# Optimization experiments

Hardware: AMD Instinct MI355X
Metric: run time of the kernel (lower is better)

Reference implementation:

```python
import jax, jax.numpy as jnp
import numpy as np
from jax import lax

B, H, W = 512, 128, 128
ARCH = [1, 4096, 4096, 4096, 4096]
CONV_THRESH = 0.0
GRAPH_THRESH = 0.8
EMBED_DIM = 1


def setup_inputs() -> dict:
    key = jax.random.key(0)
    ks = jax.random.split(key, 16)
    inp = {
        "x": jax.random.normal(ks[0], (B, 1, H, W), dtype=jnp.float32),
        "conv_w": jax.random.normal(ks[1], (1, 1, 2, 2), dtype=jnp.float32) * 0.5,
        "conv_b": jax.random.normal(ks[2], (1,), dtype=jnp.float32) * 0.1,
        "rotation": jax.random.normal(ks[3], (EMBED_DIM, EMBED_DIM), dtype=jnp.float32),
        "entangle": jax.random.normal(ks[4], (EMBED_DIM, EMBED_DIM), dtype=jnp.float32),
    }
    # Linear params, torch convention W: [out_f, in_f]
    for i, (fi, fo) in enumerate(zip(ARCH[:-1], ARCH[1:])):
        inp[f"W{i+1}"] = jax.random.normal(ks[5 + 2 * i], (fo, fi), dtype=jnp.float32) / np.sqrt(fi)
        inp[f"b{i+1}"] = jax.random.normal(ks[6 + 2 * i], (fo,), dtype=jnp.float32) * 0.01
    return inp


def _forward(x, conv_w, conv_b, rotation, entangle, W1, b1, W2, b2, W3, b3, W4, b4):
    # ConvFilter: 2x2 valid conv, sigmoid(logits - thresh), mean over C,H,W -> [B]
    logits = lax.conv_general_dilated(
        x, conv_w, window_strides=(1, 1), padding="VALID",
        dimension_numbers=("NCHW", "OIHW", "NCHW"))
    logits = logits + conv_b.reshape(1, -1, 1, 1)
    conv_out = jax.nn.sigmoid(logits - CONV_THRESH).mean(axis=(1, 2, 3))  # [B]
    conv_vec = conv_out[:, None]  # [B, 1] -> embed_dim forced to 1

    # ClassicalSelfAttention (embed_dim = 1)
    q = conv_vec @ rotation                      # [B, 1]
    k = conv_vec @ entangle                      # [B, 1]
    scores = jax.nn.softmax((q @ k.T) / np.sqrt(EMBED_DIM).astype(np.float32), axis=-1)  # [B, B]
    attn_out = scores @ conv_vec                 # [B, 1]

    # tanh MLP stack
    out = attn_out
    acts = []
    for Wl, bl in ((W1, b1), (W2, b2), (W3, b3), (W4, b4)):
        out = jnp.tanh(out @ Wl.T + bl)          # [B, out_f]
        acts.append(out)

    # Vectorized fidelity adjacency over equal-shaped layer activations:
    # normalized Gram matrix squared, thresholded (replaces the O(L^2)
    # Python loop with .item() syncs in the source).
    S = jnp.stack([a.reshape(-1) for a in acts])                  # [L, B*4096]
    S_hat = S / (jnp.linalg.norm(S, axis=1, keepdims=True) + 1e-12)
    fid = (S_hat @ S_hat.T) ** 2                                   # [L, L]
    L = len(acts)
    weights = jnp.where(fid >= GRAPH_THRESH, 1.0, 0.0) * (1.0 - jnp.eye(L, dtype=fid.dtype))
    return out, weights


def reference(x, conv_w, conv_b, rotation, entangle, W1, b1, W2, b2, W3, b3, W4, b4):
    return _forward(x, conv_w, conv_b, rotation, entangle, W1, b1, W2, b2, W3, b3, W4, b4)
```

## Files before the change

### kernel.cpp

```cpp
#include <hip/hip_runtime.h>
#include <cmath>


#define NEL (512 * 4096)

typedef float  floatx4 __attribute__((ext_vector_type(4)));
typedef _Float16 halfx8 __attribute__((ext_vector_type(8)));

__global__ __launch_bounds__(256) void conv_mean_kernel(
    const float* __restrict__ x, const float* __restrict__ cw,
    const float* __restrict__ cb, float* __restrict__ c_out)
{
  __shared__ float sbuf[4];
  const int b = blockIdx.x;
  const float w00 = cw[0], w01 = cw[1], w10 = cw[2], w11 = cw[3];
  const float bias = cb[0];
  const float* xb = x + (size_t)b * 128 * 128;
  float acc = 0.f;
  for (int t = threadIdx.x; t < 127 * 32; t += 256) {
    const int i  = t >> 5;
    const int j0 = (t & 31) << 2;
    const float* pr0 = xb + i * 128 + j0;
    const float* pr1 = pr0 + 128;
    const float4 a4 = *reinterpret_cast<const float4*>(pr0);
    const float  a5 = pr0[4];
    const float4 b4 = *reinterpret_cast<const float4*>(pr1);
    const float  b5 = pr1[4];
    const float a[5] = {a4.x, a4.y, a4.z, a4.w, a5};
    const float bb[5] = {b4.x, b4.y, b4.z, b4.w, b5};
    #pragma unroll
    for (int m = 0; m < 4; ++m) {
      if (j0 + m < 127) {
        float v = w00 * a[m] + w01 * a[m + 1] + w10 * bb[m] + w11 * bb[m + 1] + bias;
        acc += 1.0f / (1.0f + __expf(-v));
      }
    }
  }
  #pragma unroll
  for (int off = 32; off > 0; off >>= 1) acc += __shfl_down(acc, off, 64);
  const int lane = threadIdx.x & 63, wv = threadIdx.x >> 6;
  if (lane == 0) sbuf[wv] = acc;
  __syncthreads();
  if (threadIdx.x == 0)
    c_out[b] = (sbuf[0] + sbuf[1] + sbuf[2] + sbuf[3]) * (1.0f / 16129.0f);
}

__global__ __launch_bounds__(64) void attn_kernel(
    const float* __restrict__ c, const float* __restrict__ rot,
    const float* __restrict__ ent, float* __restrict__ attn)
{
  const int i = blockIdx.x;
  const int lane = threadIdx.x;
  const float t = rot[0] * ent[0] * c[i];
  float vals[8], cj[8];
  float mx = -1e30f;
  #pragma unroll
  for (int u = 0; u < 8; ++u) {
    float cv = c[lane + u * 64];
    cj[u] = cv;
    vals[u] = t * cv;
    mx = fmaxf(mx, vals[u]);
  }
  #pragma unroll
  for (int off = 32; off > 0; off >>= 1) mx = fmaxf(mx, __shfl_down(mx, off, 64));
  mx = __shfl(mx, 0, 64);
  float se = 0.f, sw = 0.f;
  #pragma unroll
  for (int u = 0; u < 8; ++u) {
    float e = __expf(vals[u] - mx);
    se += e;
    sw += e * cj[u];
  }
  #pragma unroll
  for (int off = 32; off > 0; off >>= 1) {
    se += __shfl_down(se, off, 64);
    sw += __shfl_down(sw, off, 64);
  }
  if (lane == 0) attn[i] = sw / se;
}

__global__ __launch_bounds__(256) void layer1_kernel(
    const float* __restrict__ attn, const float* __restrict__ W1,
    const float* __restrict__ b1, float* __restrict__ act1)
{
  const int o = blockIdx.x * 256 + threadIdx.x;
  const int i = blockIdx.y;
  act1[(size_t)i * 4096 + o] = tanhf(attn[i] * W1[o] + b1[o]);
}

#define BM 128
#define BN 128
#define BK 32
#define LDK 40

template<bool FUSE>
__global__ __launch_bounds__(256, 4) void gemm_tanh_kernel(
    const float* __restrict__ A, const float* __restrict__ W,
    const float* __restrict__ bias, float* __restrict__ C)
{
  __shared__ _Float16 As[2][BM][LDK];
  __shared__ _Float16 Ws[2][BN][LDK];
  const int K = 4096, N = 4096;
  const int tid  = threadIdx.x;
  const int lane = tid & 63;
  const int wave = tid >> 6;
  const int wm = (wave >> 1) * 64;
  const int wn = (wave & 1) * 64;
  const int q  = lane >> 4;
  const int ml = lane & 15;
  const int tileM = blockIdx.y * BM;
  const int tileN = blockIdx.x * BN;
  const int Kslice = K / gridDim.z;
  const int kbeg = blockIdx.z * Kslice;
  const int kend = kbeg + Kslice;
  float* Cb = FUSE ? C : C + (size_t)blockIdx.z * NEL;

  floatx4 acc[4][4] = {};

  const int r0  = tid >> 2;
  const int cc0 = (tid & 3) << 3;

  float4 pa[4], pw[4];
  auto load_tile = [&](int k0) {
    #pragma unroll
    for (int u = 0; u < 2; ++u) {
      const float* ap = A + (size_t)(tileM + r0 + u * 64) * K + k0 + cc0;
      pa[2 * u]     = *reinterpret_cast<const float4*>(ap);
      pa[2 * u + 1] = *reinterpret_cast<const float4*>(ap + 4);
      const float* wp = W + (size_t)(tileN + r0 + u * 64) * K + k0 + cc0;
      pw[2 * u]     = *reinterpret_cast<const float4*>(wp);
      pw[2 * u + 1] = *reinterpret_cast<const float4*>(wp + 4);
    }
  };
  auto store_tile = [&](int buf) {
    #pragma unroll
    for (int u = 0; u < 2; ++u) {
      halfx8 ha = { (_Float16)pa[2*u].x, (_Float16)pa[2*u].y,
                    (_Float16)pa[2*u].z, (_Float16)pa[2*u].w,
                    (_Float16)pa[2*u+1].x, (_Float16)pa[2*u+1].y,
                    (_Float16)pa[2*u+1].z, (_Float16)pa[2*u+1].w };
      *reinterpret_cast<halfx8*>(&As[buf][r0 + u * 64][cc0]) = ha;
      halfx8 hw = { (_Float16)pw[2*u].x, (_Float16)pw[2*u].y,
                    (_Float16)pw[2*u].z, (_Float16)pw[2*u].w,
                    (_Float16)pw[2*u+1].x, (_Float16)pw[2*u+1].y,
                    (_Float16)pw[2*u+1].z, (_Float16)pw[2*u+1].w };
      *reinterpret_cast<halfx8*>(&Ws[buf][r0 + u * 64][cc0]) = hw;
    }
  };

  load_tile(kbeg);
  store_tile(0);
  int cur = 0;

  for (int k0 = kbeg; k0 < kend; k0 += BK) {
    const bool more = (k0 + BK < kend);
    if (more) load_tile(k0 + BK);
    __syncthreads();

    halfx8 af[4], bf[4];
    #pragma unroll
    for (int i = 0; i < 4; ++i)
      af[i] = *reinterpret_cast<const halfx8*>(&As[cur][wm + i * 16 + ml][q * 8]);
    #pragma unroll
    for (int j = 0; j < 4; ++j)
      bf[j] = *reinterpret_cast<const halfx8*>(&Ws[cur][wn + j * 16 + ml][q * 8]);

    #pragma unroll
    for (int i = 0; i < 4; ++i)
      #pragma unroll
      for (int j = 0; j < 4; ++j)
        acc[i][j] = __builtin_amdgcn_mfma_f32_16x16x32_f16(af[i], bf[j], acc[i][j], 0, 0, 0);

    if (more) store_tile(cur ^ 1);
    cur ^= 1;
  }

  #pragma unroll
  for (int i = 0; i < 4; ++i) {
    const int row0 = tileM + wm + i * 16 + q * 4;
    #pragma unroll
    for (int j = 0; j < 4; ++j) {
      const int col = tileN + wn + j * 16 + ml;
      if (FUSE) {
        const float bv = bias[col];
        #pragma unroll
        for (int r = 0; r < 4; ++r)
          Cb[(size_t)(row0 + r) * N + col] = tanhf(acc[i][j][r] + bv);
      } else {
        #pragma unroll
        for (int r = 0; r < 4; ++r)
          Cb[(size_t)(row0 + r) * N + col] = acc[i][j][r];
      }
    }
  }
}

template<int S>
__global__ __launch_bounds__(256) void combine_tanh_kernel(
    const float* __restrict__ part, const float* __restrict__ bias,
    float* __restrict__ outp)
{
  const int i4 = blockIdx.x * 256 + threadIdx.x;
  const floatx4* p4 = (const floatx4*)part;
  floatx4 s = p4[i4];
  #pragma unroll
  for (int z = 1; z < S; ++z) s += p4[(size_t)z * (NEL / 4) + i4];
  const floatx4 bv = ((const floatx4*)bias)[i4 & 1023];
  floatx4 o;
  #pragma unroll
  for (int r = 0; r < 4; ++r) o[r] = tanhf(s[r] + bv[r]);
  ((floatx4*)outp)[i4] = o;
}

__global__ __launch_bounds__(256) void fid_dots_kernel(
    const float* __restrict__ a1, const float* __restrict__ a2,
    const float* __restrict__ a3, const float* __restrict__ a4,
    float* __restrict__ D)
{
  __shared__ float sred[4][10];
  float s[10] = {0, 0, 0, 0, 0, 0, 0, 0, 0, 0};
  const int n4 = NEL / 4;
  const int stride = gridDim.x * blockDim.x;
  const floatx4* p1 = (const floatx4*)a1;
  const floatx4* p2 = (const floatx4*)a2;
  const floatx4* p3 = (const floatx4*)a3;
  const floatx4* p4 = (const floatx4*)a4;
  for (int i = blockIdx.x * 256 + threadIdx.x; i < n4; i += stride) {
    floatx4 v1 = p1[i], v2 = p2[i], v3 = p3[i], v4 = p4[i];
    #pragma unroll
    for (int r = 0; r < 4; ++r) {
      s[0] += v1[r] * v1[r]; s[1] += v1[r] * v2[r]; s[2] += v1[r] * v3[r];
      s[3] += v1[r] * v4[r]; s[4] += v2[r] * v2[r]; s[5] += v2[r] * v3[r];
      s[6] += v2[r] * v4[r]; s[7] += v3[r] * v3[r]; s[8] += v3[r] * v4[r];
      s[9] += v4[r] * v4[r];
    }
  }
  const int lane = threadIdx.x & 63, wv = threadIdx.x >> 6;
  #pragma unroll
  for (int p = 0; p < 10; ++p) {
    float v = s[p];
    #pragma unroll
    for (int off = 32; off > 0; off >>= 1) v += __shfl_down(v, off, 64);
    if (lane == 0) sred[wv][p] = v;
  }
  __syncthreads();
  if (threadIdx.x < 10) {
    float v = sred[0][threadIdx.x] + sred[1][threadIdx.x] +
              sred[2][threadIdx.x] + sred[3][threadIdx.x];
    atomicAdd(&D[threadIdx.x * 16], v);
  }
}

__global__ void finalize_kernel(const float* __restrict__ D, float* __restrict__ wout)
{
  const int i = threadIdx.x;
  if (i >= 16) return;
  const int p = i >> 2, qq = i & 3;
  const int a = p < qq ? p : qq;
  const int b = p < qq ? qq : p;
  const int base[4] = {0, 4, 7, 9};
  const float dpq = D[(base[a] + (b - a)) * 16];
  const float npv = sqrtf(D[base[p] * 16]) + 1e-12f;
  const float nqv = sqrtf(D[base[qq] * 16]) + 1e-12f;
  const float ch = dpq / (npv * nqv);
  const float fid = ch * ch;
  wout[i] = (fid >= 0.8f && p != qq) ? 1.0f : 0.0f;
}

extern "C" void kernel_launch(void* const* d_in, const int* in_sizes, int n_in,
                              void* d_out, int out_size, void* d_ws, size_t ws_size,
                              hipStream_t stream)
{
  const float* x   = (const float*)d_in[0];
  const float* cw  = (const float*)d_in[1];
  const float* cb  = (const float*)d_in[2];
  const float* rot = (const float*)d_in[3];
  const float* ent = (const float*)d_in[4];
  const float* W1  = (const float*)d_in[5];
  const float* b1  = (const float*)d_in[6];
  const float* W2  = (const float*)d_in[7];
  const float* b2  = (const float*)d_in[8];
  const float* W3  = (const float*)d_in[9];
  const float* b3  = (const float*)d_in[10];
  const float* W4  = (const float*)d_in[11];
  const float* b4  = (const float*)d_in[12];
  float* out = (float*)d_out;

  char*  ws    = (char*)d_ws;
  float* c_buf = (float*)(ws + 0);
  float* attn  = (float*)(ws + 2048);
  float* D     = (float*)(ws + 4096);
  float* act1  = (float*)(ws + 8192);
  float* act2  = act1 + NEL;
  float* act3  = act2 + NEL;
  float* part  = act3 + NEL;
  float* wout  = out + NEL;

  const size_t base_need = 8192 + (size_t)3 * NEL * 4;
  const bool sk8 = ws_size >= base_need + (size_t)8 * NEL * 4;
  const bool sk4 = ws_size >= base_need + (size_t)4 * NEL * 4;

  hipMemsetAsync(D, 0, 10 * 16 * sizeof(float), stream);
  conv_mean_kernel<<<512, 256, 0, stream>>>(x, cw, cb, c_buf);
  attn_kernel<<<512, 64, 0, stream>>>(c_buf, rot, ent, attn);
  layer1_kernel<<<dim3(16, 512), 256, 0, stream>>>(attn, W1, b1, act1);

  const int cgrid = NEL / 4 / 256;
  if (sk8) {
    dim3 g(4096 / BN, 512 / BM, 8);
    gemm_tanh_kernel<false><<<g, 256, 0, stream>>>(act1, W2, nullptr, part);
    combine_tanh_kernel<8><<<cgrid, 256, 0, stream>>>(part, b2, act2);
    gemm_tanh_kernel<false><<<g, 256, 0, stream>>>(act2, W3, nullptr, part);
    combine_tanh_kernel<8><<<cgrid, 256, 0, stream>>>(part, b3, act3);
    gemm_tanh_kernel<false><<<g, 256, 0, stream>>>(act3, W4, nullptr, part);
    combine_tanh_kernel<8><<<cgrid, 256, 0, stream>>>(part, b4, out);
  } else if (sk4) {
    dim3 g(4096 / BN, 512 / BM, 4);
    gemm_tanh_kernel<false><<<g, 256, 0, stream>>>(act1, W2, nullptr, part);
    combine_tanh_kernel<4><<<cgrid, 256, 0, stream>>>(part, b2, act2);
    gemm_tanh_kernel<false><<<g, 256, 0, stream>>>(act2, W3, nullptr, part);
    combine_tanh_kernel<4><<<cgrid, 256, 0, stream>>>(part, b3, act3);
    gemm_tanh_kernel<false><<<g, 256, 0, stream>>>(act3, W4, nullptr, part);
    combine_tanh_kernel<4><<<cgrid, 256, 0, stream>>>(part, b4, out);
  } else {
    dim3 g(4096 / BN, 512 / BM, 1);
    gemm_tanh_kernel<true><<<g, 256, 0, stream>>>(act1, W2, b2, act2);
    gemm_tanh_kernel<true><<<g, 256, 0, stream>>>(act2, W3, b3, act3);
    gemm_tanh_kernel<true><<<g, 256, 0, stream>>>(act3, W4, b4, out);
  }

  fid_dots_kernel<<<256, 256, 0, stream>>>(act1, act2, act3, out, D);
  finalize_kernel<<<1, 64, 0, stream>>>(D, wout);
}
```

Before: 422.7 us.

## Load GEMM operands directly from global into registers with fp16 activation copies

The GEMM kernel no longer stages tiles through LDS. Each wave loads its MFMA fragments straight from global memory, register double-buffered over two k-steps. The earlier layers now also write an fp16 copy of each activation, so the A operand is read at half the bytes. The 8-way split-K path is removed in favour of a 4-way split, and launch bounds drop to 2 blocks per CU. The aim is to cut LDS traffic and barriers, at the cost of extra fp16 stores, uncoalesced strided row reads across lanes, more register pressure, and lost tile reuse within each block.

Result: slower. 517.3 us (+22.4%).

```diff
diff --git a/kernel.cpp b/kernel.cpp
--- a/kernel.cpp
+++ b/kernel.cpp
@@ -6,6 +6,7 @@
 
 typedef float  floatx4 __attribute__((ext_vector_type(4)));
 typedef _Float16 halfx8 __attribute__((ext_vector_type(8)));
+typedef _Float16 halfx4 __attribute__((ext_vector_type(4)));
 
 __global__ __launch_bounds__(256) void conv_mean_kernel(
     const float* __restrict__ x, const float* __restrict__ cw,
@@ -81,26 +82,23 @@
 
 __global__ __launch_bounds__(256) void layer1_kernel(
     const float* __restrict__ attn, const float* __restrict__ W1,
-    const float* __restrict__ b1, float* __restrict__ act1)
+    const float* __restrict__ b1, float* __restrict__ act1,
+    _Float16* __restrict__ a1h)
 {
   const int o = blockIdx.x * 256 + threadIdx.x;
   const int i = blockIdx.y;
-  act1[(size_t)i * 4096 + o] = tanhf(attn[i] * W1[o] + b1[o]);
-}
-
-#define BM 128
-#define BN 128
-#define BK 32
-#define LDK 40
+  const float v = tanhf(attn[i] * W1[o] + b1[o]);
+  act1[(size_t)i * 4096 + o] = v;
+  a1h[(size_t)i * 4096 + o] = (_Float16)v;
+}
 
 template<bool FUSE>
-__global__ __launch_bounds__(256, 4) void gemm_tanh_kernel(
-    const float* __restrict__ A, const float* __restrict__ W,
-    const float* __restrict__ bias, float* __restrict__ C)
-{
-  __shared__ _Float16 As[2][BM][LDK];
-  __shared__ _Float16 Ws[2][BN][LDK];
-  const int K = 4096, N = 4096;
+__global__ __launch_bounds__(256, 2) void gemm_direct_kernel(
+    const _Float16* __restrict__ A16, const float* __restrict__ W,
+    const float* __restrict__ bias, float* __restrict__ C,
+    _Float16* __restrict__ Ch)
+{
+  constexpr int K = 4096, N = 4096;
   const int tid  = threadIdx.x;
   const int lane = tid & 63;
   const int wave = tid >> 6;
@@ -108,71 +106,57 @@
   const int wn = (wave & 1) * 64;
   const int q  = lane >> 4;
   const int ml = lane & 15;
-  const int tileM = blockIdx.y * BM;
-  const int tileN = blockIdx.x * BN;
+  const int tileM = blockIdx.y * 128;
+  const int tileN = blockIdx.x * 128;
   const int Kslice = K / gridDim.z;
   const int kbeg = blockIdx.z * Kslice;
   const int kend = kbeg + Kslice;
   float* Cb = FUSE ? C : C + (size_t)blockIdx.z * NEL;
 
+  const _Float16* Abase = A16 + (size_t)(tileM + wm + ml) * K + q * 8;
+  const float*    Wbase = W   + (size_t)(tileN + wn + ml) * K + q * 8;
+
   floatx4 acc[4][4] = {};
-
-  const int r0  = tid >> 2;
-  const int cc0 = (tid & 3) << 3;
-
-  float4 pa[4], pw[4];
-  auto load_tile = [&](int k0) {
-    #pragma unroll
-    for (int u = 0; u < 2; ++u) {
-      const float* ap = A + (size_t)(tileM + r0 + u * 64) * K + k0 + cc0;
-      pa[2 * u]     = *reinterpret_cast<const float4*>(ap);
-      pa[2 * u + 1] = *reinterpret_cast<const float4*>(ap + 4);
-      const float* wp = W + (size_t)(tileN + r0 + u * 64) * K + k0 + cc0;
-      pw[2 * u]     = *reinterpret_cast<const float4*>(wp);
-      pw[2 * u + 1] = *reinterpret_cast<const float4*>(wp + 4);
+  halfx8 af0[4], af1[4];
+  float4 wf0[4][2], wf1[4][2];
+
+  auto loadA = [&](halfx8 (&af)[4], int k0) {
+    #pragma unroll
+    for (int i = 0; i < 4; ++i)
+      af[i] = *reinterpret_cast<const halfx8*>(Abase + (size_t)i * 16 * K + k0);
+  };
+  auto loadW = [&](float4 (&wf)[4][2], int k0) {
+    #pragma unroll
+    for (int j = 0; j < 4; ++j) {
+      const float* p = Wbase + (size_t)j * 16 * K + k0;
+      wf[j][0] = *reinterpret_cast<const float4*>(p);
+      wf[j][1] = *reinterpret_cast<const float4*>(p + 4);
     }
   };
-  auto store_tile = [&](int buf) {
-    #pragma unroll
-    for (int u = 0; u < 2; ++u) {
-      halfx8 ha = { (_Float16)pa[2*u].x, (_Float16)pa[2*u].y,
-                    (_Float16)pa[2*u].z, (_Float16)pa[2*u].w,
-                    (_Float16)pa[2*u+1].x, (_Float16)pa[2*u+1].y,
-                    (_Float16)pa[2*u+1].z, (_Float16)pa[2*u+1].w };
-      *reinterpret_cast<halfx8*>(&As[buf][r0 + u * 64][cc0]) = ha;
-      halfx8 hw = { (_Float16)pw[2*u].x, (_Float16)pw[2*u].y,
-                    (_Float16)pw[2*u].z, (_Float16)pw[2*u].w,
-                    (_Float16)pw[2*u+1].x, (_Float16)pw[2*u+1].y,
-                    (_Float16)pw[2*u+1].z, (_Float16)pw[2*u+1].w };
-      *reinterpret_cast<halfx8*>(&Ws[buf][r0 + u * 64][cc0]) = hw;
-    }
-  };
-
-  load_tile(kbeg);
-  store_tile(0);
-  int cur = 0;
-
-  for (int k0 = kbeg; k0 < kend; k0 += BK) {
-    const bool more = (k0 + BK < kend);
-    if (more) load_tile(k0 + BK);
-    __syncthreads();
-
-    halfx8 af[4], bf[4];
-    #pragma unroll
-    for (int i = 0; i < 4; ++i)
-      af[i] = *reinterpret_cast<const halfx8*>(&As[cur][wm + i * 16 + ml][q * 8]);
+  auto consume = [&](halfx8 (&af)[4], float4 (&wf)[4][2]) {
+    halfx8 bf[4];
     #pragma unroll
     for (int j = 0; j < 4; ++j)
-      bf[j] = *reinterpret_cast<const halfx8*>(&Ws[cur][wn + j * 16 + ml][q * 8]);
-
+      bf[j] = halfx8{ (_Float16)wf[j][0].x, (_Float16)wf[j][0].y,
+                      (_Float16)wf[j][0].z, (_Float16)wf[j][0].w,
+                      (_Float16)wf[j][1].x, (_Float16)wf[j][1].y,
+                      (_Float16)wf[j][1].z, (_Float16)wf[j][1].w };
     #pragma unroll
     for (int i = 0; i < 4; ++i)
       #pragma unroll
       for (int j = 0; j < 4; ++j)
         acc[i][j] = __builtin_amdgcn_mfma_f32_16x16x32_f16(af[i], bf[j], acc[i][j], 0, 0, 0);
-
-    if (more) store_tile(cur ^ 1);
-    cur ^= 1;
+  };
+
+  loadA(af0, kbeg);
+  loadW(wf0, kbeg);
+  for (int k0 = kbeg; k0 < kend; k0 += 64) {
+    const bool m1 = (k0 + 32) < kend;
+    const bool m2 = (k0 + 64) < kend;
+    if (m1) { loadA(af1, k0 + 32); loadW(wf1, k0 + 32); }
+    consume(af0, wf0);
+    if (m2) { loadA(af0, k0 + 64); loadW(wf0, k0 + 64); }
+    if (m1) consume(af1, wf1);
   }
 
   #pragma unroll
@@ -184,8 +168,11 @@
       if (FUSE) {
         const float bv = bias[col];
         #pragma unroll
-        for (int r = 0; r < 4; ++r)
-          Cb[(size_t)(row0 + r) * N + col] = tanhf(acc[i][j][r] + bv);
+        for (int r = 0; r < 4; ++r) {
+          const float v = tanhf(acc[i][j][r] + bv);
+          Cb[(size_t)(row0 + r) * N + col] = v;
+          if (Ch) Ch[(size_t)(row0 + r) * N + col] = (_Float16)v;
+        }
       } else {
         #pragma unroll
         for (int r = 0; r < 4; ++r)
@@ -195,10 +182,10 @@
   }
 }
 
-template<int S>
+template<int S, bool H>
 __global__ __launch_bounds__(256) void combine_tanh_kernel(
     const float* __restrict__ part, const float* __restrict__ bias,
-    float* __restrict__ outp)
+    float* __restrict__ outp, _Float16* __restrict__ houtp)
 {
   const int i4 = blockIdx.x * 256 + threadIdx.x;
   const floatx4* p4 = (const floatx4*)part;
@@ -210,6 +197,10 @@
   #pragma unroll
   for (int r = 0; r < 4; ++r) o[r] = tanhf(s[r] + bv[r]);
   ((floatx4*)outp)[i4] = o;
+  if (H) {
+    halfx4 h = { (_Float16)o[0], (_Float16)o[1], (_Float16)o[2], (_Float16)o[3] };
+    ((halfx4*)houtp)[i4] = h;
+  }
 }
 
 __global__ __launch_bounds__(256) void fid_dots_kernel(
@@ -293,40 +284,34 @@
   float* act1  = (float*)(ws + 8192);
   float* act2  = act1 + NEL;
   float* act3  = act2 + NEL;
-  float* part  = act3 + NEL;
+  _Float16* a1h = (_Float16*)(act3 + NEL);
+  _Float16* a2h = a1h + NEL;
+  _Float16* a3h = a2h + NEL;
+  float* part  = (float*)(a3h + NEL);
   float* wout  = out + NEL;
 
-  const size_t base_need = 8192 + (size_t)3 * NEL * 4;
-  const bool sk8 = ws_size >= base_need + (size_t)8 * NEL * 4;
+  const size_t base_need = 8192 + (size_t)3 * NEL * 4 + (size_t)3 * NEL * 2;
   const bool sk4 = ws_size >= base_need + (size_t)4 * NEL * 4;
 
   hipMemsetAsync(D, 0, 10 * 16 * sizeof(float), stream);
   conv_mean_kernel<<<512, 256, 0, stream>>>(x, cw, cb, c_buf);
   attn_kernel<<<512, 64, 0, stream>>>(c_buf, rot, ent, attn);
-  layer1_kernel<<<dim3(16, 512), 256, 0, stream>>>(attn, W1, b1, act1);
+  layer1_kernel<<<dim3(16, 512), 256, 0, stream>>>(attn, W1, b1, act1, a1h);
 
   const int cgrid = NEL / 4 / 256;
-  if (sk8) {
-    dim3 g(4096 / BN, 512 / BM, 8);
-    gemm_tanh_kernel<false><<<g, 256, 0, stream>>>(act1, W2, nullptr, part);
-    combine_tanh_kernel<8><<<cgrid, 256, 0, stream>>>(part, b2, act2);
-    gemm_tanh_kernel<false><<<g, 256, 0, stream>>>(act2, W3, nullptr, part);
-    combine_tanh_kernel<8><<<cgrid, 256, 0, stream>>>(part, b3, act3);
-    gemm_tanh_kernel<false><<<g, 256, 0, stream>>>(act3, W4, nullptr, part);
-    combine_tanh_kernel<8><<<cgrid, 256, 0, stream>>>(part, b4, out);
-  } else if (sk4) {
-    dim3 g(4096 / BN, 512 / BM, 4);
-    gemm_tanh_kernel<false><<<g, 256, 0, stream>>>(act1, W2, nullptr, part);
-    combine_tanh_kernel<4><<<cgrid, 256, 0, stream>>>(part, b2, act2);
-    gemm_tanh_kernel<false><<<g, 256, 0, stream>>>(act2, W3, nullptr, part);
-    combine_tanh_kernel<4><<<cgrid, 256, 0, stream>>>(part, b3, act3);
-    gemm_tanh_kernel<false><<<g, 256, 0, stream>>>(act3, W4, nullptr, part);
-    combine_tanh_kernel<4><<<cgrid, 256, 0, stream>>>(part, b4, out);
+  if (sk4) {
+    dim3 g(32, 4, 4);
+    gemm_direct_kernel<false><<<g, 256, 0, stream>>>(a1h, W2, nullptr, part, nullptr);
+    combine_tanh_kernel<4, true><<<cgrid, 256, 0, stream>>>(part, b2, act2, a2h);
+    gemm_direct_kernel<false><<<g, 256, 0, stream>>>(a2h, W3, nullptr, part, nullptr);
+    combine_tanh_kernel<4, true><<<cgrid, 256, 0, stream>>>(part, b3, act3, a3h);
+    gemm_direct_kernel<false><<<g, 256, 0, stream>>>(a3h, W4, nullptr, part, nullptr);
+    combine_tanh_kernel<4, false><<<cgrid, 256, 0, stream>>>(part, b4, out, nullptr);
   } else {
-    dim3 g(4096 / BN, 512 / BM, 1);
-    gemm_tanh_kernel<true><<<g, 256, 0, stream>>>(act1, W2, b2, act2);
-    gemm_tanh_kernel<true><<<g, 256, 0, stream>>>(act2, W3, b3, act3);
-    gemm_tanh_kernel<true><<<g, 256, 0, stream>>>(act3, W4, b4, out);
+    dim3 g(32, 4, 1);
+    gemm_direct_kernel<true><<<g, 256, 0, stream>>>(a1h, W2, b2, act2, a2h);
+    gemm_direct_kernel<true><<<g, 256, 0, stream>>>(a2h, W3, b3, act3, a3h);
+    gemm_direct_kernel<true><<<g, 256, 0, stream>>>(a3h, W4, b4, out, nullptr);
   }
 
   fid_dots_kernel<<<256, 256, 0, stream>>>(act1, act2, act3, out, D);
```

## Swizzle LDS tiles, fuse attention with layer1, hardcode split-K 8 path

Applied to the files above, without the earlier changes.

Replaces the padded LDS layout (LDK 40) with an unpadded XOR-swizzled layout, shrinking shared memory while avoiding bank conflicts on the MFMA fragment reads. Replaces __syncthreads with an explicit lgkmcnt wait plus s_barrier, so the barrier no longer waits on outstanding global prefetch loads. Fuses the attention softmax and the layer-1 tanh into one kernel, removing a launch and the attn round trip. The workspace-size fallbacks are dropped and split-K 8 is hardcoded, which could fault if the workspace is smaller than that path needs.

After: 423.5 us. No clear change (+0.2%).

```diff
diff --git a/kernel.cpp b/kernel.cpp
--- a/kernel.cpp
+++ b/kernel.cpp
@@ -6,6 +6,11 @@
 
 typedef float  floatx4 __attribute__((ext_vector_type(4)));
 typedef _Float16 halfx8 __attribute__((ext_vector_type(8)));
+
+#define BM 128
+#define BN 128
+#define BK 32
+#define LDK 32
 
 __global__ __launch_bounds__(256) void conv_mean_kernel(
     const float* __restrict__ x, const float* __restrict__ cw,
@@ -45,58 +50,54 @@
     c_out[b] = (sbuf[0] + sbuf[1] + sbuf[2] + sbuf[3]) * (1.0f / 16129.0f);
 }
 
-__global__ __launch_bounds__(64) void attn_kernel(
+__global__ __launch_bounds__(256) void attn_layer1_kernel(
     const float* __restrict__ c, const float* __restrict__ rot,
-    const float* __restrict__ ent, float* __restrict__ attn)
-{
+    const float* __restrict__ ent, const float* __restrict__ W1,
+    const float* __restrict__ b1, float* __restrict__ act1)
+{
+  __shared__ float sattn;
   const int i = blockIdx.x;
-  const int lane = threadIdx.x;
-  const float t = rot[0] * ent[0] * c[i];
-  float vals[8], cj[8];
-  float mx = -1e30f;
-  #pragma unroll
-  for (int u = 0; u < 8; ++u) {
-    float cv = c[lane + u * 64];
-    cj[u] = cv;
-    vals[u] = t * cv;
-    mx = fmaxf(mx, vals[u]);
-  }
-  #pragma unroll
-  for (int off = 32; off > 0; off >>= 1) mx = fmaxf(mx, __shfl_down(mx, off, 64));
-  mx = __shfl(mx, 0, 64);
-  float se = 0.f, sw = 0.f;
-  #pragma unroll
-  for (int u = 0; u < 8; ++u) {
-    float e = __expf(vals[u] - mx);
-    se += e;
-    sw += e * cj[u];
-  }
-  #pragma unroll
-  for (int off = 32; off > 0; off >>= 1) {
-    se += __shfl_down(se, off, 64);
-    sw += __shfl_down(sw, off, 64);
-  }
-  if (lane == 0) attn[i] = sw / se;
-}
-
-__global__ __launch_bounds__(256) void layer1_kernel(
-    const float* __restrict__ attn, const float* __restrict__ W1,
-    const float* __restrict__ b1, float* __restrict__ act1)
-{
-  const int o = blockIdx.x * 256 + threadIdx.x;
-  const int i = blockIdx.y;
-  act1[(size_t)i * 4096 + o] = tanhf(attn[i] * W1[o] + b1[o]);
-}
-
-#define BM 128
-#define BN 128
-#define BK 32
-#define LDK 40
-
-template<bool FUSE>
-__global__ __launch_bounds__(256, 4) void gemm_tanh_kernel(
+  if (threadIdx.x < 64) {
+    const int lane = threadIdx.x;
+    const float t = rot[0] * ent[0] * c[i];
+    float vals[8], cj[8];
+    float mx = -1e30f;
+    #pragma unroll
+    for (int u = 0; u < 8; ++u) {
+      float cv = c[lane + u * 64];
+      cj[u] = cv;
+      vals[u] = t * cv;
+      mx = fmaxf(mx, vals[u]);
+    }
+    #pragma unroll
+    for (int off = 32; off > 0; off >>= 1) mx = fmaxf(mx, __shfl_down(mx, off, 64));
+    mx = __shfl(mx, 0, 64);
+    float se = 0.f, sw = 0.f;
+    #pragma unroll
+    for (int u = 0; u < 8; ++u) {
+      float e = __expf(vals[u] - mx);
+      se += e;
+      sw += e * cj[u];
+    }
+    #pragma unroll
+    for (int off = 32; off > 0; off >>= 1) {
+      se += __shfl_down(se, off, 64);
+      sw += __shfl_down(sw, off, 64);
+    }
+    if (lane == 0) sattn = sw / se;
+  }
+  __syncthreads();
+  const float av = sattn;
+  #pragma unroll
+  for (int k = 0; k < 16; ++k) {
+    const int o = k * 256 + threadIdx.x;
+    act1[(size_t)i * 4096 + o] = tanhf(av * W1[o] + b1[o]);
+  }
+}
+
+__global__ __launch_bounds__(256, 4) void gemm_kernel(
     const float* __restrict__ A, const float* __restrict__ W,
-    const float* __restrict__ bias, float* __restrict__ C)
+    float* __restrict__ part)
 {
   __shared__ _Float16 As[2][BM][LDK];
   __shared__ _Float16 Ws[2][BN][LDK];
@@ -110,24 +111,25 @@
   const int ml = lane & 15;
   const int tileM = blockIdx.y * BM;
   const int tileN = blockIdx.x * BN;
-  const int Kslice = K / gridDim.z;
-  const int kbeg = blockIdx.z * Kslice;
-  const int kend = kbeg + Kslice;
-  float* Cb = FUSE ? C : C + (size_t)blockIdx.z * NEL;
+  const int kbeg = blockIdx.z * 512;
+  const int kend = kbeg + 512;
+  float* Cb = part + (size_t)blockIdx.z * NEL;
 
   floatx4 acc[4][4] = {};
 
-  const int r0  = tid >> 2;
-  const int cc0 = (tid & 3) << 3;
+  const int r0 = tid >> 2;
+  const int u0 = tid & 3;
+  const int su0 = (u0 ^ (r0 & 3)) << 3;
+  const int sq = (q ^ (ml & 3)) << 3;
 
   float4 pa[4], pw[4];
   auto load_tile = [&](int k0) {
     #pragma unroll
     for (int u = 0; u < 2; ++u) {
-      const float* ap = A + (size_t)(tileM + r0 + u * 64) * K + k0 + cc0;
+      const float* ap = A + (size_t)(tileM + r0 + u * 64) * K + k0 + u0 * 8;
       pa[2 * u]     = *reinterpret_cast<const float4*>(ap);
       pa[2 * u + 1] = *reinterpret_cast<const float4*>(ap + 4);
-      const float* wp = W + (size_t)(tileN + r0 + u * 64) * K + k0 + cc0;
+      const float* wp = W + (size_t)(tileN + r0 + u * 64) * K + k0 + u0 * 8;
       pw[2 * u]     = *reinterpret_cast<const float4*>(wp);
       pw[2 * u + 1] = *reinterpret_cast<const float4*>(wp + 4);
     }
@@ -139,12 +141,12 @@
                     (_Float16)pa[2*u].z, (_Float16)pa[2*u].w,
                     (_Float16)pa[2*u+1].x, (_Float16)pa[2*u+1].y,
                     (_Float16)pa[2*u+1].z, (_Float16)pa[2*u+1].w };
-      *reinterpret_cast<halfx8*>(&As[buf][r0 + u * 64][cc0]) = ha;
+      *reinterpret_cast<halfx8*>(&As[buf][r0 + u * 64][su0]) = ha;
       halfx8 hw = { (_Float16)pw[2*u].x, (_Float16)pw[2*u].y,
                     (_Float16)pw[2*u].z, (_Float16)pw[2*u].w,
                     (_Float16)pw[2*u+1].x, (_Float16)pw[2*u+1].y,
                     (_Float16)pw[2*u+1].z, (_Float16)pw[2*u+1].w };
-      *reinterpret_cast<halfx8*>(&Ws[buf][r0 + u * 64][cc0]) = hw;
+      *reinterpret_cast<halfx8*>(&Ws[buf][r0 + u * 64][su0]) = hw;
     }
   };
 
@@ -155,15 +157,17 @@
   for (int k0 = kbeg; k0 < kend; k0 += BK) {
     const bool more = (k0 + BK < kend);
     if (more) load_tile(k0 + BK);
-    __syncthreads();
+
+    asm volatile("s_waitcnt lgkmcnt(0)" ::: "memory");
+    __builtin_amdgcn_s_barrier();
 
     halfx8 af[4], bf[4];
     #pragma unroll
     for (int i = 0; i < 4; ++i)
-      af[i] = *reinterpret_cast<const halfx8*>(&As[cur][wm + i * 16 + ml][q * 8]);
+      af[i] = *reinterpret_cast<const halfx8*>(&As[cur][wm + i * 16 + ml][sq]);
     #pragma unroll
     for (int j = 0; j < 4; ++j)
-      bf[j] = *reinterpret_cast<const halfx8*>(&Ws[cur][wn + j * 16 + ml][q * 8]);
+      bf[j] = *reinterpret_cast<const halfx8*>(&Ws[cur][wn + j * 16 + ml][sq]);
 
     #pragma unroll
     for (int i = 0; i < 4; ++i)
@@ -181,21 +185,13 @@
     #pragma unroll
     for (int j = 0; j < 4; ++j) {
       const int col = tileN + wn + j * 16 + ml;
-      if (FUSE) {
-        const float bv = bias[col];
-        #pragma unroll
-        for (int r = 0; r < 4; ++r)
-          Cb[(size_t)(row0 + r) * N + col] = tanhf(acc[i][j][r] + bv);
-      } else {
-        #pragma unroll
-        for (int r = 0; r < 4; ++r)
-          Cb[(size_t)(row0 + r) * N + col] = acc[i][j][r];
-      }
-    }
-  }
-}
-
-template<int S>
+      #pragma unroll
+      for (int r = 0; r < 4; ++r)
+        Cb[(size_t)(row0 + r) * N + col] = acc[i][j][r];
+    }
+  }
+}
+
 __global__ __launch_bounds__(256) void combine_tanh_kernel(
     const float* __restrict__ part, const float* __restrict__ bias,
     float* __restrict__ outp)
@@ -204,7 +200,7 @@
   const floatx4* p4 = (const floatx4*)part;
   floatx4 s = p4[i4];
   #pragma unroll
-  for (int z = 1; z < S; ++z) s += p4[(size_t)z * (NEL / 4) + i4];
+  for (int z = 1; z < 8; ++z) s += p4[(size_t)z * (NEL / 4) + i4];
   const floatx4 bv = ((const floatx4*)bias)[i4 & 1023];
   floatx4 o;
   #pragma unroll
@@ -288,7 +284,6 @@
 
   char*  ws    = (char*)d_ws;
   float* c_buf = (float*)(ws + 0);
-  float* attn  = (float*)(ws + 2048);
   float* D     = (float*)(ws + 4096);
   float* act1  = (float*)(ws + 8192);
   float* act2  = act1 + NEL;
@@ -296,38 +291,18 @@
   float* part  = act3 + NEL;
   float* wout  = out + NEL;
 
-  const size_t base_need = 8192 + (size_t)3 * NEL * 4;
-  const bool sk8 = ws_size >= base_need + (size_t)8 * NEL * 4;
-  const bool sk4 = ws_size >= base_need + (size_t)4 * NEL * 4;
-
   hipMemsetAsync(D, 0, 10 * 16 * sizeof(float), stream);
   conv_mean_kernel<<<512, 256, 0, stream>>>(x, cw, cb, c_buf);
-  attn_kernel<<<512, 64, 0, stream>>>(c_buf, rot, ent, attn);
-  layer1_kernel<<<dim3(16, 512), 256, 0, stream>>>(attn, W1, b1, act1);
+  attn_layer1_kernel<<<512, 256, 0, stream>>>(c_buf, rot, ent, W1, b1, act1);
 
   const int cgrid = NEL / 4 / 256;
-  if (sk8) {
-    dim3 g(4096 / BN, 512 / BM, 8);
-    gemm_tanh_kernel<false><<<g, 256, 0, stream>>>(act1, W2, nullptr, part);
-    combine_tanh_kernel<8><<<cgrid, 256, 0, stream>>>(part, b2, act2);
-    gemm_tanh_kernel<false><<<g, 256, 0, stream>>>(act2, W3, nullptr, part);
-    combine_tanh_kernel<8><<<cgrid, 256, 0, stream>>>(part, b3, act3);
-    gemm_tanh_kernel<false><<<g, 256, 0, stream>>>(act3, W4, nullptr, part);
-    combine_tanh_kernel<8><<<cgrid, 256, 0, stream>>>(part, b4, out);
-  } else if (sk4) {
-    dim3 g(4096 / BN, 512 / BM, 4);
-    gemm_tanh_kernel<false><<<g, 256, 0, stream>>>(act1, W2, nullptr, part);
-    combine_tanh_kernel<4><<<cgrid, 256, 0, stream>>>(part, b2, act2);
-    gemm_tanh_kernel<false><<<g, 256, 0, stream>>>(act2, W3, nullptr, part);
-    combine_tanh_kernel<4><<<cgrid, 256, 0, stream>>>(part, b3, act3);
-    gemm_tanh_kernel<false><<<g, 256, 0, stream>>>(act3, W4, nullptr, part);
-    combine_tanh_kernel<4><<<cgrid, 256, 0, stream>>>(part, b4, out);
-  } else {
-    dim3 g(4096 / BN, 512 / BM, 1);
-    gemm_tanh_kernel<true><<<g, 256, 0, stream>>>(act1, W2, b2, act2);
-    gemm_tanh_kernel<true><<<g, 256, 0, stream>>>(act2, W3, b3, act3);
-    gemm_tanh_kernel<true><<<g, 256, 0, stream>>>(act3, W4, b4, out);
-  }
+  dim3 g(32, 4, 8);
+  gemm_kernel<<<g, 256, 0, stream>>>(act1, W2, part);
+  combine_tanh_kernel<<<cgrid, 256, 0, stream>>>(part, b2, act2);
+  gemm_kernel<<<g, 256, 0, stream>>>(act2, W3, part);
+  combine_tanh_kernel<<<cgrid, 256, 0, stream>>>(part, b3, act3);
+  gemm_kernel<<<g, 256, 0, stream>>>(act3, W4, part);
+  combine_tanh_kernel<<<cgrid, 256, 0, stream>>>(part, b4, out);
 
   fid_dots_kernel<<<256, 256, 0, stream>>>(act1, act2, act3, out, D);
   finalize_kernel<<<1, 64, 0, stream>>>(D, wout);
```
